# Optimization experiments

Hardware: AMD Instinct MI355X
Metric: run time of the kernel (lower is better)

Reference implementation:

```python
import jax, jax.numpy as jnp
import numpy as np

B, S, D, H, DFF = 2, 2048, 1024, 16, 4096
DH = D // H
EPS = 1e-12


def _layer_norm(x, g, b):
    mu = jnp.mean(x, axis=-1, keepdims=True)
    var = jnp.mean(jnp.square(x - mu), axis=-1, keepdims=True)
    return (x - mu) * jax.lax.rsqrt(var + EPS) * g + b


def setup_inputs() -> dict:
    key = jax.random.key(0)
    ks = jax.random.split(key, 12)
    s = 0.02
    return {
        "query": jax.random.normal(ks[0], (B, S, D), jnp.float32),
        "key_in": jax.random.normal(ks[1], (B, S, D), jnp.float32),
        "value_in": jax.random.normal(ks[2], (B, S, D), jnp.float32),
        "attention_mask": jnp.zeros((B, 1, 1, S), jnp.float32),
        # weights stored [in, out] (i.e., torch Linear weight transposed)
        "Wq": jax.random.normal(ks[3], (D, D), jnp.float32) * s,
        "bq": jnp.zeros((D,), jnp.float32),
        "Wk": jax.random.normal(ks[4], (D, D), jnp.float32) * s,
        "bk": jnp.zeros((D,), jnp.float32),
        "Wv": jax.random.normal(ks[5], (D, D), jnp.float32) * s,
        "bv": jnp.zeros((D,), jnp.float32),
        "Wo": jax.random.normal(ks[6], (D, D), jnp.float32) * s,
        "bo": jnp.zeros((D,), jnp.float32),
        "ln1_g": jnp.ones((D,), jnp.float32),
        "ln1_b": jnp.zeros((D,), jnp.float32),
        "Wi": jax.random.normal(ks[7], (D, DFF), jnp.float32) * s,
        "bi": jnp.zeros((DFF,), jnp.float32),
        "Wd": jax.random.normal(ks[8], (DFF, D), jnp.float32) * s,
        "bd": jnp.zeros((D,), jnp.float32),
        "ln2_g": jnp.ones((D,), jnp.float32),
        "ln2_b": jnp.zeros((D,), jnp.float32),
    }


def reference(query, key_in, value_in, attention_mask, Wq, bq, Wk, bk, Wv, bv,
              Wo, bo, ln1_g, ln1_b, Wi, bi, Wd, bd, ln2_g, ln2_b):
    # projections -> [B, H, S, DH]
    q = (query @ Wq + bq).reshape(B, S, H, DH).transpose(0, 2, 1, 3)
    k = (key_in @ Wk + bk).reshape(B, S, H, DH).transpose(0, 2, 1, 3)
    v = (value_in @ Wv + bv).reshape(B, S, H, DH).transpose(0, 2, 1, 3)
    # eager attention: full [B,H,S,S] score matrix, as in the source
    scores = jnp.einsum("bhqd,bhkd->bhqk", q, k) / jnp.sqrt(jnp.float32(DH))
    scores = scores + attention_mask
    probs = jax.nn.softmax(scores, axis=-1)  # dropout p=0 -> identity
    ctx = jnp.einsum("bhqk,bhkd->bhqd", probs, v)
    ctx = ctx.transpose(0, 2, 1, 3).reshape(B, S, D)
    attn_out = ctx @ Wo + bo
    attn_out = _layer_norm(attn_out + query, ln1_g, ln1_b)
    inter = jax.nn.gelu(attn_out @ Wi + bi, approximate=False)
    layer_out = inter @ Wd + bd
    return _layer_norm(layer_out + attn_out, ln2_g, ln2_b)
```

## Files before the change

### kernel.cpp

```cpp
#include <hip/hip_runtime.h>
#include <hip/hip_bf16.h>
#include <cmath>

#define B_   2
#define S_   2048
#define D_   1024
#define H_   16
#define DFF_ 4096
#define DH_  64
#define M_   (B_*S_)

typedef __bf16 bfx8 __attribute__((ext_vector_type(8)));
typedef __bf16 bfx4 __attribute__((ext_vector_type(4)));
typedef float  fx4  __attribute__((ext_vector_type(4)));

__device__ __forceinline__ float fast_exp2(float x) {
  float r;
  asm volatile("v_exp_f32 %0, %1" : "=v"(r) : "v"(x));
  return r;
}

__device__ __forceinline__ float fast_erf(float x) {
  float ax = fabsf(x);
  float t  = __builtin_amdgcn_rcpf(fmaf(0.3275911f, ax, 1.0f));
  float p  = fmaf(1.061405429f, t, -1.453152027f);
  p = fmaf(p, t, 1.421413741f);
  p = fmaf(p, t, -0.284496736f);
  p = fmaf(p, t, 0.254829592f);
  p = p * t;
  float e  = fast_exp2(-ax * ax * 1.44269504f);
  float r  = 1.0f - p * e;
  return copysignf(r, x);
}

__device__ __forceinline__ void gload_lds16(const void* g, void* l) {
  __builtin_amdgcn_global_load_lds((__attribute__((address_space(1))) void*)(g),
                                   (__attribute__((address_space(3))) void*)(l),
                                   16, 0, 0);
}

struct PrepArgs {
  const float* win[6]; __bf16* wout[6];
  const float* cin[3]; __bf16* cout[3];
};

__global__ __launch_bounds__(256)
void prep_kernel(PrepArgs a) {
  int bid = blockIdx.x;
  if (bid < 12288) {
    __shared__ float t[32][33];
    int wsel, tr, tc, R, C;
    if (bid < 4096) {
      wsel = bid >> 10; int l = bid & 1023;
      tr = l >> 5; tc = l & 31; R = D_; C = D_;
    } else if (bid < 8192) {
      wsel = 4; int l = bid - 4096;
      tr = l >> 7; tc = l & 127; R = D_; C = DFF_;
    } else {
      wsel = 5; int l = bid - 8192;
      tr = l >> 5; tc = l & 31; R = DFF_; C = D_;
    }
    const float* in = a.win[wsel];
    __bf16* out = a.wout[wsel];
    int r0 = tr * 32, c0 = tc * 32;
    int tx = threadIdx.x & 31, ty = threadIdx.x >> 5;
#pragma unroll
    for (int j = 0; j < 4; ++j) {
      int r = ty + j * 8;
      t[r][tx] = in[(size_t)(r0 + r) * C + c0 + tx];
    }
    __syncthreads();
#pragma unroll
    for (int j = 0; j < 4; ++j) {
      int c = ty + j * 8;
      out[(size_t)(c0 + c) * R + r0 + tx] = (__bf16)t[tx][c];
    }
  } else {
    int l = bid - 12288;
    int z = l >> 12;
    int i = ((l & 4095) * 256 + threadIdx.x) * 4;
    float4 v = *(const float4*)(a.cin[z] + i);
    bfx4 o;
    o[0] = (__bf16)v.x; o[1] = (__bf16)v.y; o[2] = (__bf16)v.z; o[3] = (__bf16)v.w;
    *(bfx4*)(a.cout[z] + i) = o;
  }
}

__global__ __launch_bounds__(256)
void transpose_v_kernel(const __bf16* __restrict__ vb, __bf16* __restrict__ vt) {
  __shared__ __bf16 t[32][33];
  int bh = blockIdx.z;
  int b = bh >> 4, h = bh & 15;
  int s0 = blockIdx.x * 32, d0 = blockIdx.y * 32;
  int tx = threadIdx.x, ty = threadIdx.y;
#pragma unroll
  for (int j = 0; j < 4; ++j) {
    int s = ty + j * 8;
    t[s][tx] = vb[(size_t)((b * S_ + s0 + s) * H_ + h) * DH_ + d0 + tx];
  }
  __syncthreads();
#pragma unroll
  for (int j = 0; j < 4; ++j) {
    int d = ty + j * 8;
    vt[(size_t)(bh * DH_ + d0 + d) * S_ + s0 + tx] = t[tx][d];
  }
}

template<int MODE, int TBN>
__global__ __launch_bounds__(256)
void gemm_kernel(const __bf16* __restrict__ A, const __bf16* __restrict__ Bt,
                 const float* __restrict__ bias, const void* __restrict__ res,
                 void* __restrict__ out, int Ndim, int Kdim) {
  __shared__ alignas(16) __bf16 As[2 * 128 * 64];
  __shared__ alignas(16) __bf16 Bs[2 * TBN * 64];
  const int tid  = threadIdx.x;
  const int lane = tid & 63;
  const int w    = tid >> 6;
  const int wm   = w >> 1, wn = w & 1;
  constexpr int NF = TBN / 32;

  const int gX  = gridDim.x;
  const int nwg = gridDim.x * gridDim.y;
  int lid = blockIdx.y * gX + blockIdx.x;
  int swz = (lid & 7) * (nwg >> 3) + (lid >> 3);
  const int m0 = (swz / gX) * 128, n0 = (swz % gX) * TBN;

  fx4 acc[4][NF];
#pragma unroll
  for (int i = 0; i < 4; ++i)
#pragma unroll
    for (int j = 0; j < NF; ++j) acc[i][j] = {0.f, 0.f, 0.f, 0.f};

  const int KT = Kdim / 64;

  auto stage = [&](int kt, int buf) {
    const int kb0 = kt * 64;
#pragma unroll
    for (int i = 0; i < 4; ++i) {
      int o   = tid * 16 + i * 4096;
      int row = o >> 7, cb = o & 127;
      int cbs = cb ^ ((row & 7) << 4);
      gload_lds16((const char*)A + ((size_t)(m0 + row) * Kdim + kb0) * 2 + cbs,
                  (char*)As + buf * 16384 + o);
    }
#pragma unroll
    for (int i = 0; i < NF; ++i) {
      int o   = tid * 16 + i * 4096;
      int row = o >> 7, cb = o & 127;
      int cbs = cb ^ ((row & 7) << 4);
      gload_lds16((const char*)Bt + ((size_t)(n0 + row) * Kdim + kb0) * 2 + cbs,
                  (char*)Bs + buf * (TBN * 128) + o);
    }
  };

  stage(0, 0);
  asm volatile("s_waitcnt vmcnt(0)" ::: "memory");
  __builtin_amdgcn_s_barrier();
  __builtin_amdgcn_sched_barrier(0);

  for (int kt = 0; kt < KT; ++kt) {
    if (kt + 1 < KT) stage(kt + 1, (kt + 1) & 1);
    __builtin_amdgcn_sched_barrier(0);
    if (kt > 0) {
      if (kt + 1 < KT) {
        if constexpr (TBN == 64) asm volatile("s_waitcnt vmcnt(6)" ::: "memory");
        else                     asm volatile("s_waitcnt vmcnt(8)" ::: "memory");
      } else {
        asm volatile("s_waitcnt vmcnt(0)" ::: "memory");
      }
      __builtin_amdgcn_s_barrier();
      __builtin_amdgcn_sched_barrier(0);
    }
    const char* Ab = (const char*)As + (kt & 1) * 16384;
    const char* Bb = (const char*)Bs + (kt & 1) * (TBN * 128);

#pragma unroll
    for (int kk = 0; kk < 2; ++kk) {
      bfx8 afr[4], bfr[NF];
      const int cb = kk * 64 + ((lane >> 4) << 4);
#pragma unroll
      for (int mf = 0; mf < 4; ++mf) {
        int row = wm * 64 + mf * 16 + (lane & 15);
        afr[mf] = *(const bfx8*)(Ab + row * 128 + (cb ^ ((row & 7) << 4)));
      }
#pragma unroll
      for (int nf = 0; nf < NF; ++nf) {
        int row = wn * (TBN / 2) + nf * 16 + (lane & 15);
        bfr[nf] = *(const bfx8*)(Bb + row * 128 + (cb ^ ((row & 7) << 4)));
      }
#pragma unroll
      for (int mf = 0; mf < 4; ++mf)
#pragma unroll
        for (int nf = 0; nf < NF; ++nf)
          acc[mf][nf] = __builtin_amdgcn_mfma_f32_16x16x32_bf16(afr[mf], bfr[nf],
                                                                acc[mf][nf], 0, 0, 0);
    }
    __builtin_amdgcn_s_barrier();
    __builtin_amdgcn_sched_barrier(0);
  }

#pragma unroll
  for (int mf = 0; mf < 4; ++mf) {
#pragma unroll
    for (int nf = 0; nf < NF; ++nf) {
      int col = n0 + wn * (TBN / 2) + nf * 16 + (lane & 15);
      float bvl = bias[col];
#pragma unroll
      for (int r = 0; r < 4; ++r) {
        int rowg = m0 + wm * 64 + mf * 16 + ((lane >> 4) << 2) + r;
        float v = acc[mf][nf][r] + bvl;
        if (MODE == 2) v = 0.5f * v * (1.0f + fast_erf(v * 0.70710678118654752f));
        if (MODE == 4) v += (float)((const __bf16*)res)[(size_t)rowg * Ndim + col];
        if (MODE == 1) ((float*)out)[(size_t)rowg * Ndim + col] = v;
        else           ((__bf16*)out)[(size_t)rowg * Ndim + col] = (__bf16)v;
      }
    }
  }
}

__device__ __forceinline__ void stage_a256(const __bf16* __restrict__ A, int m0,
                                           int Kdim, int tile, int h, char* Asm) {
  char* dst = Asm + (tile & 1) * 32768;
  const int kb0 = tile * 64;
  const int tid = threadIdx.x;
#pragma unroll
  for (int it = 0; it < 2; ++it) {
    int o = tid * 16 + it * 8192;
    int lrow = o >> 7, cb = o & 127;
    int r = (lrow & 63) + h * 64 + ((lrow >> 6) << 7);
    int csrc = cb ^ ((r & 7) << 4);
    gload_lds16((const char*)A + ((size_t)(m0 + r) * Kdim + kb0) * 2 + csrc,
                dst + r * 128 + cb);
  }
}
__device__ __forceinline__ void stage_b256(const __bf16* __restrict__ Bt, int n0,
                                           int Kdim, int tile, int h, char* Bsm) {
  char* dst = Bsm + (tile & 1) * 32768;
  const int kb0 = tile * 64;
  const int tid = threadIdx.x;
#pragma unroll
  for (int it = 0; it < 2; ++it) {
    int o = tid * 16 + it * 8192;
    int lrow = o >> 7, cb = o & 127;
    int r = h * 128 + lrow;
    int csrc = cb ^ ((r & 7) << 4);
    gload_lds16((const char*)Bt + ((size_t)(n0 + r) * Kdim + kb0) * 2 + csrc,
                dst + r * 128 + cb);
  }
}

template<int MODE>
__device__ __forceinline__ void gemm256_body(const __bf16* __restrict__ A,
                                             const __bf16* __restrict__ Bt,
                                             const float* __restrict__ bias,
                                             void* __restrict__ out,
                                             int Ndim, int Kdim, int m0, int n0) {
  extern __shared__ char smem[];
  char* Asm = smem;
  char* Bsm = smem + 65536;
  const int tid  = threadIdx.x;
  const int lane = tid & 63;
  const int w    = tid >> 6;
  const int wm   = w >> 2;
  const int wn   = w & 3;
  const int g    = lane >> 4;
  const int ql   = lane & 15;
  const int KT   = Kdim / 64;

  fx4 acc[8][4];
#pragma unroll
  for (int i = 0; i < 8; ++i)
#pragma unroll
    for (int j = 0; j < 4; ++j) acc[i][j] = {0.f, 0.f, 0.f, 0.f};

  stage_a256(A, m0, Kdim, 0, 0, Asm);
  stage_a256(A, m0, Kdim, 0, 1, Asm);
  stage_b256(Bt, n0, Kdim, 0, 0, Bsm);
  stage_b256(Bt, n0, Kdim, 0, 1, Bsm);
  stage_a256(A, m0, Kdim, 1, 0, Asm);
  asm volatile("s_waitcnt vmcnt(2)" ::: "memory");
  __builtin_amdgcn_s_barrier();
  __builtin_amdgcn_sched_barrier(0);

  for (int t = 0; t < KT; ++t) {
    const char* Ab = Asm + (t & 1) * 32768;
    const char* Bb = Bsm + (t & 1) * 32768;
#pragma unroll
    for (int p = 0; p < 4; ++p) {
      const int ah = p >> 1, kk = p & 1;
      if (p == 0 && t + 1 < KT) stage_a256(A, m0, Kdim, t + 1, 1, Asm);
      if (p == 1 && t + 1 < KT) stage_b256(Bt, n0, Kdim, t + 1, 0, Bsm);
      if (p == 2 && t + 1 < KT) stage_b256(Bt, n0, Kdim, t + 1, 1, Bsm);
      if (p == 3 && t + 2 < KT) stage_a256(A, m0, Kdim, t + 2, 0, Asm);
      __builtin_amdgcn_sched_barrier(0);

      bfx8 af[4], bf[4];
      const int cbv = kk * 64 + g * 16;
#pragma unroll
      for (int j = 0; j < 4; ++j) {
        int arow = wm * 128 + (ah * 4 + j) * 16 + ql;
        af[j] = *(const bfx8*)(Ab + arow * 128 + (cbv ^ ((arow & 7) << 4)));
      }
#pragma unroll
      for (int nf = 0; nf < 4; ++nf) {
        int brow = wn * 64 + nf * 16 + ql;
        bf[nf] = *(const bfx8*)(Bb + brow * 128 + (cbv ^ ((brow & 7) << 4)));
      }
      __builtin_amdgcn_sched_barrier(0);
      __builtin_amdgcn_s_barrier();
      asm volatile("s_waitcnt lgkmcnt(0)" ::: "memory");
      __builtin_amdgcn_sched_barrier(0);
      __builtin_amdgcn_s_setprio(1);
#pragma unroll
      for (int j = 0; j < 4; ++j)
#pragma unroll
        for (int nf = 0; nf < 4; ++nf)
          acc[ah * 4 + j][nf] = __builtin_amdgcn_mfma_f32_16x16x32_bf16(
              af[j], bf[nf], acc[ah * 4 + j][nf], 0, 0, 0);
      __builtin_amdgcn_s_setprio(0);
      __builtin_amdgcn_s_barrier();
      __builtin_amdgcn_sched_barrier(0);
    }
    if (t + 1 < KT) {
      if (t + 2 < KT) asm volatile("s_waitcnt vmcnt(2)" ::: "memory");
      else            asm volatile("s_waitcnt vmcnt(0)" ::: "memory");
      __builtin_amdgcn_s_barrier();
      __builtin_amdgcn_sched_barrier(0);
    }
  }

#pragma unroll
  for (int mf = 0; mf < 8; ++mf) {
#pragma unroll
    for (int nf = 0; nf < 4; ++nf) {
      int col = n0 + wn * 64 + nf * 16 + ql;
      float bvl = bias[col];
#pragma unroll
      for (int r = 0; r < 4; ++r) {
        int rowg = m0 + wm * 128 + mf * 16 + g * 4 + r;
        float v = acc[mf][nf][r] + bvl;
        if (MODE == 2) v = 0.5f * v * (1.0f + fast_erf(v * 0.70710678118654752f));
        if (MODE == 1) ((float*)out)[(size_t)rowg * Ndim + col] = v;
        else          ((__bf16*)out)[(size_t)rowg * Ndim + col] = (__bf16)v;
      }
    }
  }
}

template<int MODE>
__global__ __launch_bounds__(512)
void gemm256_kernel(const __bf16* __restrict__ A, const __bf16* __restrict__ Bt,
                    const float* __restrict__ bias, void* __restrict__ out,
                    int Ndim, int Kdim) {
  const int gX  = gridDim.x;
  const int nwg = gridDim.x * gridDim.y;
  int lid = blockIdx.y * gX + blockIdx.x;
  int swz = (lid & 7) * (nwg >> 3) + (lid >> 3);
  gemm256_body<MODE>(A, Bt, bias, out, Ndim, Kdim,
                     (swz / gX) * 256, (swz % gX) * 256);
}

struct QKVArgs {
  const __bf16* A[3]; const __bf16* Bt[3]; const float* bias[3]; __bf16* out[3];
};

__global__ __launch_bounds__(512)
void qkv256_kernel(QKVArgs args, int Ndim, int Kdim) {
  int z = blockIdx.z;
  gemm256_body<0>(args.A[z], args.Bt[z], args.bias[z], (void*)args.out[z],
                  Ndim, Kdim, blockIdx.y * 256, blockIdx.x * 256);
}

__global__ __launch_bounds__(512)
void attn_kernel(const __bf16* __restrict__ Qb, const __bf16* __restrict__ Kb,
                 const __bf16* __restrict__ Vt, const float* __restrict__ mask,
                 __bf16* __restrict__ ctx) {
  __shared__ alignas(16) __bf16 Ks[3 * 64 * 64];
  __shared__ alignas(16) __bf16 Vs[3 * 64 * 64];
  __shared__ alignas(16) __bf16 Ps[8 * 16 * 64];
  __shared__ alignas(16) float  Ms[2048];

  const int tid  = threadIdx.x;
  const int lane = tid & 63;
  const int w    = tid >> 6;
  const int g    = lane >> 4;
  const int ql   = lane & 15;
  const int bh   = blockIdx.y;
  const int b    = bh >> 4;
  const int h    = bh & 15;
  const int q0   = blockIdx.x * 128;

  const size_t kbase  = ((size_t)(b * S_)) * D_ + h * DH_;
  const size_t vtbase = (size_t)bh * DH_ * S_;
  const int NT = S_ / 64;

  char* Qsm = (char*)Ps;
  const size_t qbase = ((size_t)(b * S_) + q0) * D_ + h * DH_;
#pragma unroll
  for (int i = 0; i < 2; ++i) {
    int o   = tid * 16 + i * 8192;
    int row = o >> 7, cb = o & 127;
    int cbs = cb ^ ((row & 7) << 4);
    gload_lds16((const char*)Qb + (qbase + (size_t)row * D_) * 2 + cbs, Qsm + o);
  }
  {
    int o = tid * 16;
    gload_lds16((const char*)mask + (size_t)b * S_ * 4 + o, (char*)Ms + o);
  }
  {
    int o   = tid * 16;
    int row = o >> 7, cb = o & 127;
    int cbs = cb ^ ((row & 7) << 4);
    gload_lds16((const char*)Kb + (kbase + (size_t)row * D_) * 2 + cbs, (char*)Ks + o);
    gload_lds16((const char*)Vt + (vtbase + (size_t)row * S_) * 2 + cbs, (char*)Vs + o);
    gload_lds16((const char*)Kb + (kbase + (size_t)(64 + row) * D_) * 2 + cbs,
                (char*)Ks + 8192 + o);
    gload_lds16((const char*)Vt + (vtbase + (size_t)row * S_ + 64) * 2 + cbs,
                (char*)Vs + 8192 + o);
  }
  asm volatile("s_waitcnt vmcnt(4)" ::: "memory");
  __builtin_amdgcn_s_barrier();
  __builtin_amdgcn_sched_barrier(0);

  {
    float4 mv = *(float4*)((char*)Ms + tid * 16);
    mv.x *= 1.44269504f; mv.y *= 1.44269504f;
    mv.z *= 1.44269504f; mv.w *= 1.44269504f;
    *(float4*)((char*)Ms + tid * 16) = mv;
  }

  bfx8 aq[2];
  {
    int row = w * 16 + ql;
#pragma unroll
    for (int kk = 0; kk < 2; ++kk) {
      int cb = kk * 64 + g * 16;
      aq[kk] = *(const bfx8*)(Qsm + row * 128 + (cb ^ ((row & 7) << 4)));
    }
  }
  __syncthreads();
  asm volatile("s_waitcnt vmcnt(2)" ::: "memory");
  __builtin_amdgcn_s_barrier();
  __builtin_amdgcn_sched_barrier(0);

  fx4 acc[4];
  fx4 accl = {0.f, 0.f, 0.f, 0.f};
#pragma unroll
  for (int d = 0; d < 4; ++d) acc[d] = {0.f, 0.f, 0.f, 0.f};

  bfx8 ones;
#pragma unroll
  for (int j = 0; j < 8; ++j) ones[j] = (__bf16)1.0f;

  char* pw = (char*)Ps + w * 2048;
  const float SCL = 0.18033688f;

  for (int t = 0; t < NT; ++t) {
    const int kv0 = t * 64;
    if (t + 2 < NT) {
      int o   = tid * 16;
      int row = o >> 7, cb = o & 127;
      int cbs = cb ^ ((row & 7) << 4);
      int nkv = kv0 + 128;
      int bo  = ((t + 2) % 3) * 8192;
      gload_lds16((const char*)Kb + (kbase + (size_t)(nkv + row) * D_) * 2 + cbs,
                  (char*)Ks + bo + o);
      gload_lds16((const char*)Vt + (vtbase + (size_t)row * S_ + nkv) * 2 + cbs,
                  (char*)Vs + bo + o);
    }
    __builtin_amdgcn_sched_barrier(0);
    const char* Kc = (const char*)Ks + (t % 3) * 8192;
    const char* Vc = (const char*)Vs + (t % 3) * 8192;

    fx4 sc[4];
#pragma unroll
    for (int nf = 0; nf < 4; ++nf) sc[nf] = {0.f, 0.f, 0.f, 0.f};
#pragma unroll
    for (int kk = 0; kk < 2; ++kk) {
      const int cb = kk * 64 + g * 16;
      bfx8 bk[4];
#pragma unroll
      for (int nf = 0; nf < 4; ++nf) {
        int row = nf * 16 + ql;
        bk[nf] = *(const bfx8*)(Kc + row * 128 + (cb ^ ((row & 7) << 4)));
      }
      __builtin_amdgcn_s_setprio(1);
#pragma unroll
      for (int nf = 0; nf < 4; ++nf)
        sc[nf] = __builtin_amdgcn_mfma_f32_16x16x32_bf16(bk[nf], aq[kk], sc[nf], 0, 0, 0);
      __builtin_amdgcn_s_setprio(0);
    }

    float sv[4][4];
#pragma unroll
    for (int nf = 0; nf < 4; ++nf) {
      float4 mk = *(const float4*)((const char*)Ms + (kv0 + nf * 16 + g * 4) * 4);
      sv[nf][0] = fast_exp2(fmaf(sc[nf][0], SCL, mk.x));
      sv[nf][1] = fast_exp2(fmaf(sc[nf][1], SCL, mk.y));
      sv[nf][2] = fast_exp2(fmaf(sc[nf][2], SCL, mk.z));
      sv[nf][3] = fast_exp2(fmaf(sc[nf][3], SCL, mk.w));
    }

#pragma unroll
    for (int nf = 0; nf < 4; ++nf) {
      bfx4 pv;
      pv[0] = (__bf16)sv[nf][0]; pv[1] = (__bf16)sv[nf][1];
      pv[2] = (__bf16)sv[nf][2]; pv[3] = (__bf16)sv[nf][3];
      int c = (nf * 32 + g * 8) ^ ((ql & 7) << 4);
      *(bfx4*)(pw + ql * 128 + c) = pv;
    }

    asm volatile("s_waitcnt lgkmcnt(0)" ::: "memory");
    __builtin_amdgcn_sched_barrier(0);

#pragma unroll
    for (int kk = 0; kk < 2; ++kk) {
      int prow = ql;
      int cb   = kk * 64 + g * 16;
      bfx8 ap  = *(const bfx8*)((const char*)pw + prow * 128 + (cb ^ ((prow & 7) << 4)));
      __builtin_amdgcn_s_setprio(1);
#pragma unroll
      for (int d = 0; d < 4; ++d) {
        int vrow = d * 16 + ql;
        bfx8 bv  = *(const bfx8*)(Vc + vrow * 128 + (cb ^ ((vrow & 7) << 4)));
        acc[d] = __builtin_amdgcn_mfma_f32_16x16x32_bf16(ap, bv, acc[d], 0, 0, 0);
      }
      accl = __builtin_amdgcn_mfma_f32_16x16x32_bf16(ap, ones, accl, 0, 0, 0);
      __builtin_amdgcn_s_setprio(0);
    }

    if (t + 1 < NT) {
      if (t + 2 < NT) asm volatile("s_waitcnt vmcnt(2)" ::: "memory");
      else            asm volatile("s_waitcnt vmcnt(0)" ::: "memory");
      __builtin_amdgcn_s_barrier();
      __builtin_amdgcn_sched_barrier(0);
    }
  }

#pragma unroll
  for (int r = 0; r < 4; ++r) {
    float inv = 1.0f / accl[r];
    int qrow = q0 + w * 16 + g * 4 + r;
    size_t base = ((size_t)(b * S_) + qrow) * D_ + h * DH_;
#pragma unroll
    for (int d = 0; d < 4; ++d)
      ctx[base + d * 16 + ql] = (__bf16)(acc[d][r] * inv);
  }
}

template<bool WRITE_BF16>
__global__ __launch_bounds__(256)
void ln_kernel(const __bf16* __restrict__ a,
               const float* __restrict__ g, const float* __restrict__ beta,
               float* __restrict__ outf, __bf16* __restrict__ outb) {
  const int row = blockIdx.x;
  const int tid = threadIdx.x;
  const size_t base = (size_t)row * D_;
  bfx4 xa = *(const bfx4*)(a + base + tid * 4);
  float x[4] = {(float)xa[0], (float)xa[1], (float)xa[2], (float)xa[3]};
  float s = x[0] + x[1] + x[2] + x[3];
#pragma unroll
  for (int m = 1; m < 64; m <<= 1) s += __shfl_xor(s, m);
  __shared__ float red[8];
  if ((tid & 63) == 0) red[tid >> 6] = s;
  __syncthreads();
  float mu = (red[0] + red[1] + red[2] + red[3]) * (1.0f / D_);
  float v0 = 0.f;
#pragma unroll
  for (int i = 0; i < 4; ++i) { float d = x[i] - mu; v0 += d * d; }
#pragma unroll
  for (int m = 1; m < 64; m <<= 1) v0 += __shfl_xor(v0, m);
  if ((tid & 63) == 0) red[4 + (tid >> 6)] = v0;
  __syncthreads();
  float var = (red[4] + red[5] + red[6] + red[7]) * (1.0f / D_);
  float rs = rsqrtf(var + 1e-12f);
#pragma unroll
  for (int i = 0; i < 4; ++i) {
    int col = tid * 4 + i;
    x[i] = (x[i] - mu) * rs * g[col] + beta[col];
  }
  if (WRITE_BF16) {
    bfx4 o;
    o[0] = (__bf16)x[0]; o[1] = (__bf16)x[1]; o[2] = (__bf16)x[2]; o[3] = (__bf16)x[3];
    *(bfx4*)(outb + base + tid * 4) = o;
  } else {
    *(float4*)(outf + base + tid * 4) = make_float4(x[0], x[1], x[2], x[3]);
  }
}

extern "C" void kernel_launch(void* const* d_in, const int* in_sizes, int n_in,
                              void* d_out, int out_size, void* d_ws, size_t ws_size,
                              hipStream_t stream) {
  const float* query    = (const float*)d_in[0];
  const float* key_in   = (const float*)d_in[1];
  const float* value_in = (const float*)d_in[2];
  const float* mask     = (const float*)d_in[3];
  const float* Wq = (const float*)d_in[4];  const float* bq = (const float*)d_in[5];
  const float* Wk = (const float*)d_in[6];  const float* bk = (const float*)d_in[7];
  const float* Wv = (const float*)d_in[8];  const float* bv = (const float*)d_in[9];
  const float* Wo = (const float*)d_in[10]; const float* bo = (const float*)d_in[11];
  const float* ln1g = (const float*)d_in[12]; const float* ln1b = (const float*)d_in[13];
  const float* Wi = (const float*)d_in[14]; const float* bi = (const float*)d_in[15];
  const float* Wd = (const float*)d_in[16]; const float* bd = (const float*)d_in[17];
  const float* ln2g = (const float*)d_in[18]; const float* ln2b = (const float*)d_in[19];

  char* ws = (char*)d_ws;
  const size_t MB = 1ull << 20;
  if (ws_size < 112 * MB) return;

  __bf16* xq   = (__bf16*)(ws + 0 * MB);
  __bf16* xk   = (__bf16*)(ws + 8 * MB);
  __bf16* xv   = (__bf16*)(ws + 16 * MB);
  __bf16* x1b  = (__bf16*)(ws + 16 * MB);
  __bf16* qb   = (__bf16*)(ws + 24 * MB);
  __bf16* inter= (__bf16*)(ws + 24 * MB);
  __bf16* kb   = (__bf16*)(ws + 32 * MB);
  __bf16* vb   = (__bf16*)(ws + 40 * MB);
  __bf16* alinb= (__bf16*)(ws + 40 * MB);
  __bf16* vt   = (__bf16*)(ws + 48 * MB);
  __bf16* ctxb = (__bf16*)(ws + 56 * MB);
  __bf16* ffb  = (__bf16*)(ws + 56 * MB);
  __bf16* wqt  = (__bf16*)(ws + 88 * MB);
  __bf16* wkt  = (__bf16*)(ws + 90 * MB);
  __bf16* wvt  = (__bf16*)(ws + 92 * MB);
  __bf16* wot  = (__bf16*)(ws + 94 * MB);
  __bf16* wit  = (__bf16*)(ws + 96 * MB);
  __bf16* wdt  = (__bf16*)(ws + 104 * MB);

  dim3 b256(256);
  dim3 tblk(32, 8);

  PrepArgs pa;
  pa.win[0] = Wq; pa.win[1] = Wk; pa.win[2] = Wv; pa.win[3] = Wo;
  pa.win[4] = Wi; pa.win[5] = Wd;
  pa.wout[0] = wqt; pa.wout[1] = wkt; pa.wout[2] = wvt; pa.wout[3] = wot;
  pa.wout[4] = wit; pa.wout[5] = wdt;
  pa.cin[0] = query; pa.cin[1] = key_in; pa.cin[2] = value_in;
  pa.cout[0] = xq;   pa.cout[1] = xk;    pa.cout[2] = xv;
  prep_kernel<<<dim3(24576), b256, 0, stream>>>(pa);

  QKVArgs qa;
  qa.A[0] = xq;  qa.A[1] = xk;  qa.A[2] = xv;
  qa.Bt[0] = wqt; qa.Bt[1] = wkt; qa.Bt[2] = wvt;
  qa.bias[0] = bq; qa.bias[1] = bk; qa.bias[2] = bv;
  qa.out[0] = qb; qa.out[1] = kb; qa.out[2] = vb;
  qkv256_kernel<<<dim3(D_ / 256, M_ / 256, 3), dim3(512), 131072, stream>>>(qa, D_, D_);

  transpose_v_kernel<<<dim3(S_ / 32, 2, B_ * H_), tblk, 0, stream>>>(vb, vt);

  attn_kernel<<<dim3(S_ / 128, B_ * H_), dim3(512), 0, stream>>>(qb, kb, vt, mask, ctxb);

  gemm_kernel<4, 64><<<dim3(D_ / 64, M_ / 128), b256, 0, stream>>>(ctxb, wot, bo, xq, (void*)alinb, D_, D_);

  ln_kernel<true><<<dim3(M_), b256, 0, stream>>>(alinb, ln1g, ln1b, nullptr, x1b);

  gemm256_kernel<2><<<dim3(DFF_ / 256, M_ / 256), dim3(512), 131072, stream>>>(x1b, wit, bi, (void*)inter, DFF_, D_);

  gemm_kernel<4, 64><<<dim3(D_ / 64, M_ / 128), b256, 0, stream>>>(inter, wdt, bd, x1b, (void*)ffb, D_, DFF_);

  ln_kernel<false><<<dim3(M_), b256, 0, stream>>>(ffb, ln2g, ln2b, (float*)d_out, nullptr);
}
```

Before: 240.9 us.

## Software-pipeline QK^T one tile ahead of softmax and PV in attention

Computes the QK^T scores for tile t+1 while the exp/PV work for tile t runs, with a prologue that computes the scores for the first tile. The aim is to hide MFMA latency behind the exp work through cross-iteration overlap. To keep tile t+1 safe to read, the vmcnt waits are tightened from 2 to 0, which shrinks the prefetch depth so global loads are no longer left in flight across the barrier. The setprio hints around the QK MFMAs are dropped, and register pressure rises from the extra score accumulators.

```diff
diff --git a/kernel.cpp b/kernel.cpp
--- a/kernel.cpp
+++ b/kernel.cpp
@@ -439,7 +439,7 @@
     }
   }
   __syncthreads();
-  asm volatile("s_waitcnt vmcnt(2)" ::: "memory");
+  asm volatile("s_waitcnt vmcnt(0)" ::: "memory");
   __builtin_amdgcn_s_barrier();
   __builtin_amdgcn_sched_barrier(0);
 
@@ -454,6 +454,23 @@
 
   char* pw = (char*)Ps + w * 2048;
   const float SCL = 0.18033688f;
+
+  fx4 scp[4];
+#pragma unroll
+  for (int nf = 0; nf < 4; ++nf) scp[nf] = {0.f, 0.f, 0.f, 0.f};
+#pragma unroll
+  for (int kk = 0; kk < 2; ++kk) {
+    const int cb = kk * 64 + g * 16;
+    bfx8 bk[4];
+#pragma unroll
+    for (int nf = 0; nf < 4; ++nf) {
+      int row = nf * 16 + ql;
+      bk[nf] = *(const bfx8*)((const char*)Ks + row * 128 + (cb ^ ((row & 7) << 4)));
+    }
+#pragma unroll
+    for (int nf = 0; nf < 4; ++nf)
+      scp[nf] = __builtin_amdgcn_mfma_f32_16x16x32_bf16(bk[nf], aq[kk], scp[nf], 0, 0, 0);
+  }
 
   for (int t = 0; t < NT; ++t) {
     const int kv0 = t * 64;
@@ -469,36 +486,36 @@
                   (char*)Vs + bo + o);
     }
     __builtin_amdgcn_sched_barrier(0);
-    const char* Kc = (const char*)Ks + (t % 3) * 8192;
     const char* Vc = (const char*)Vs + (t % 3) * 8192;
 
-    fx4 sc[4];
-#pragma unroll
-    for (int nf = 0; nf < 4; ++nf) sc[nf] = {0.f, 0.f, 0.f, 0.f};
-#pragma unroll
-    for (int kk = 0; kk < 2; ++kk) {
-      const int cb = kk * 64 + g * 16;
-      bfx8 bk[4];
-#pragma unroll
-      for (int nf = 0; nf < 4; ++nf) {
-        int row = nf * 16 + ql;
-        bk[nf] = *(const bfx8*)(Kc + row * 128 + (cb ^ ((row & 7) << 4)));
-      }
-      __builtin_amdgcn_s_setprio(1);
-#pragma unroll
-      for (int nf = 0; nf < 4; ++nf)
-        sc[nf] = __builtin_amdgcn_mfma_f32_16x16x32_bf16(bk[nf], aq[kk], sc[nf], 0, 0, 0);
-      __builtin_amdgcn_s_setprio(0);
+    fx4 scn[4];
+    if (t + 1 < NT) {
+      const char* Kn = (const char*)Ks + ((t + 1) % 3) * 8192;
+#pragma unroll
+      for (int nf = 0; nf < 4; ++nf) scn[nf] = {0.f, 0.f, 0.f, 0.f};
+#pragma unroll
+      for (int kk = 0; kk < 2; ++kk) {
+        const int cb = kk * 64 + g * 16;
+        bfx8 bk[4];
+#pragma unroll
+        for (int nf = 0; nf < 4; ++nf) {
+          int row = nf * 16 + ql;
+          bk[nf] = *(const bfx8*)(Kn + row * 128 + (cb ^ ((row & 7) << 4)));
+        }
+#pragma unroll
+        for (int nf = 0; nf < 4; ++nf)
+          scn[nf] = __builtin_amdgcn_mfma_f32_16x16x32_bf16(bk[nf], aq[kk], scn[nf], 0, 0, 0);
+      }
     }
 
     float sv[4][4];
 #pragma unroll
     for (int nf = 0; nf < 4; ++nf) {
       float4 mk = *(const float4*)((const char*)Ms + (kv0 + nf * 16 + g * 4) * 4);
-      sv[nf][0] = fast_exp2(fmaf(sc[nf][0], SCL, mk.x));
-      sv[nf][1] = fast_exp2(fmaf(sc[nf][1], SCL, mk.y));
-      sv[nf][2] = fast_exp2(fmaf(sc[nf][2], SCL, mk.z));
-      sv[nf][3] = fast_exp2(fmaf(sc[nf][3], SCL, mk.w));
+      sv[nf][0] = fast_exp2(fmaf(scp[nf][0], SCL, mk.x));
+      sv[nf][1] = fast_exp2(fmaf(scp[nf][1], SCL, mk.y));
+      sv[nf][2] = fast_exp2(fmaf(scp[nf][2], SCL, mk.z));
+      sv[nf][3] = fast_exp2(fmaf(scp[nf][3], SCL, mk.w));
     }
 
 #pragma unroll
@@ -530,7 +547,9 @@
     }
 
     if (t + 1 < NT) {
-      if (t + 2 < NT) asm volatile("s_waitcnt vmcnt(2)" ::: "memory");
+#pragma unroll
+      for (int nf = 0; nf < 4; ++nf) scp[nf] = scn[nf];
+      if (t + 2 < NT) asm volatile("s_waitcnt vmcnt(0)" ::: "memory");
       else            asm volatile("s_waitcnt vmcnt(0)" ::: "memory");
       __builtin_amdgcn_s_barrier();
       __builtin_amdgcn_sched_barrier(0);
```

Result: no change. 242.5 us (+0.7%).
